# Performance work log

Hardware: AMD Instinct MI355X
Metric: run time of the kernel (lower is better)

Reference implementation:

```python
import jax, jax.numpy as jnp
import numpy as np

ROI = 268
K = 32
SLOPE = 0.33
EPS = 1e-5

def leaky(h):
    return jnp.where(h >= 0, h, SLOPE * h)

def bn(h, g, b):
    # BatchNorm in training mode: biased batch statistics over the node/batch axis
    mu = h.mean(0)
    var = ((h - mu) ** 2).mean(0)
    return (h - mu) * jax.lax.rsqrt(var + EPS) * g + b


def setup_inputs():
    B, F, C, deg = 64, ROI, 32, 32
    N = B * ROI
    key = jax.random.key(0)
    ks = jax.random.split(key, 32)
    x = jax.random.normal(ks[0], (N, F), jnp.float32)
    # static within-graph edges: every node has exactly `deg` incoming edges
    tgt = jnp.repeat(jnp.arange(N, dtype=jnp.int32), deg)
    src = (tgt // ROI) * ROI + jax.random.randint(ks[1], (N * deg,), 0, ROI, dtype=jnp.int32)
    edge_index = jnp.stack([src, tgt])
    batch = jnp.repeat(jnp.arange(B, dtype=jnp.int32), ROI)
    def lin(k, i, o):
        return 0.05 * jax.random.normal(k, (i, o), jnp.float32)
    def vec(k, o):
        return 0.05 * jax.random.normal(k, (o,), jnp.float32)
    p = dict(
        x=x, edge_index=edge_index, batch=batch,
        W1a=lin(ks[2], 2 * F, C), b1a=vec(ks[3], C), W1b=lin(ks[4], C, C), b1b=vec(ks[5], C),
        g1=1.0 + vec(ks[6], C), be1=vec(ks[7], C),
        W2a=lin(ks[8], 2 * F, C), b2a=vec(ks[9], C), W2b=lin(ks[10], C, C), b2b=vec(ks[11], C),
        g2=1.0 + vec(ks[12], C), be2=vec(ks[13], C),
        W3=lin(ks[14], 2 * F, 1), b3=vec(ks[15], 1), g3=1.0 + vec(ks[16], 1), be3=vec(ks[17], 1),
        Wl1=lin(ks[18], ROI + 2 * C, 256), bl1=vec(ks[19], 256), g4=1.0 + vec(ks[20], 256), be4=vec(ks[21], 256),
        Wl2=lin(ks[22], 256, 128), bl2=vec(ks[23], 128), g5=1.0 + vec(ks[24], 128), be5=vec(ks[25], 128),
        Wl3=lin(ks[26], 128, 1), bl3=vec(ks[27], 1),
    )
    return p


def reference(x, edge_index, batch,
              W1a, b1a, W1b, b1b, g1, be1,
              W2a, b2a, W2b, b2b, g2, be2,
              W3, b3, g3, be3,
              Wl1, bl1, g4, be4, Wl2, bl2, g5, be5, Wl3, bl3):
    N, F = x.shape
    B = N // ROI
    src, tgt = edge_index[0], edge_index[1]
    xi = x[tgt]                       # [E, F] central node feature
    xd = x[src] - xi                  # [E, F] x_j - x_i
    # --- gcn1: EdgeConv(mlp1) + BN + LeakyReLU (dropout = identity in eval) ---
    m1 = leaky(xi @ W1a[:F] + xd @ W1a[F:] + b1a) @ W1b + b1b   # [E, C]
    a1 = jax.ops.segment_max(m1, tgt, num_segments=N)
    a1 = jnp.where(jnp.isfinite(a1), a1, 0.0)
    x1 = leaky(bn(a1, g1, be1))
    # --- gcn3: EdgeConv(mlp3) + BN + LeakyReLU ---
    m3 = xi @ W3[:F] + xd @ W3[F:] + b3                          # [E, 1]
    a3 = jax.ops.segment_max(m3, tgt, num_segments=N)
    a3 = jnp.where(jnp.isfinite(a3), a3, 0.0)
    x3 = leaky(bn(a3, g3, be3))
    # --- gcn2: DynamicEdgeConv(mlp2, k=32) + BN + LeakyReLU ---
    xg = x.reshape(B, ROI, F)
    sq = jnp.sum(xg * xg, -1)
    d2 = sq[:, :, None] + sq[:, None, :] - 2.0 * jnp.einsum('bif,bjf->bij', xg, xg)
    _, idx = jax.lax.top_k(-d2, K)                               # [B, ROI, K], includes self
    xj = jax.vmap(lambda f, i: f[i])(xg, idx)                    # [B, ROI, K, F]
    part_i = jnp.einsum('bif,fc->bic', xg, W2a[:F])
    part_d = jnp.einsum('bikf,fc->bikc', xj - xg[:, :, None, :], W2a[F:])
    h2 = leaky(part_i[:, :, None, :] + part_d + b2a)
    m2 = h2 @ W2b + b2b                                          # [B, ROI, K, C]
    x2 = leaky(bn(m2.max(axis=2).reshape(N, -1), g2, be2))
    # --- readout ---
    counts = jax.ops.segment_sum(jnp.ones((N, 1), x.dtype), batch, num_segments=B)
    p1 = jax.ops.segment_sum(x1, batch, num_segments=B) / counts
    p2 = jax.ops.segment_sum(x2, batch, num_segments=B) / counts
    z = jnp.concatenate([p1, p2, x3.reshape(B, ROI)], -1)        # [B, 268+64]
    z = leaky(bn(z @ Wl1 + bl1, g4, be4))
    z = leaky(bn(z @ Wl2 + bl2, g5, be5))
    return z @ Wl3 + bl3                                          # [B, 1]
```

## Files before the change

kernel.cpp:

```cpp
#include <hip/hip_runtime.h>
#include <hip/hip_bf16.h>

#define ROI   268
#define FDIM  268
#define NB    64
#define NN    (NB*ROI)
#define CC    32
#define DEG   32
#define KSEL  32
#define SLOPE 0.33f
#define EPSBN 1e-5f

typedef __attribute__((ext_vector_type(8)))  short bf16x8;
typedef __attribute__((ext_vector_type(4)))  float f32x4;
typedef __attribute__((ext_vector_type(16))) float f32x16;

__device__ __forceinline__ float lrelu(float h) { return h >= 0.f ? h : SLOPE * h; }

__device__ __forceinline__ unsigned short f2bf(float f) {
    union { __hip_bfloat16 h; unsigned short s; } u;
    u.h = __float2bfloat16(f);
    return u.s;
}
__device__ __forceinline__ float bf2f(unsigned short h) {
    return __uint_as_float(((unsigned int)h) << 16);
}

#define PREP_PACK_BLOCKS  2448
#define PREP_PACKW_BLOCKS 18
#define PREP_SCAL_BLOCKS  1072

__global__ __launch_bounds__(256) void k_prep(
    const float* __restrict__ x,
    const float* __restrict__ W1a, const float* __restrict__ W2a,
    const float* __restrict__ W3,  const float* __restrict__ b3,
    unsigned short* __restrict__ Xh, unsigned short* __restrict__ Xl,
    unsigned short* __restrict__ Wfh, unsigned short* __restrict__ Wfl,
    float* __restrict__ u3, float* __restrict__ v3, float* __restrict__ sqv)
{
    const int bid = blockIdx.x;
    const int tid = threadIdx.x;
    if (bid < PREP_PACK_BLOCKS) {
        const int gid = bid * 256 + tid;
        const int l   = gid & 63;
        const int f3  = gid >> 6;
        const int ks  = f3 % 9;
        const int bc  = f3 / 9;
        const int ct  = bc % 17;
        const int b   = bc / 17;
        const int node = ct * 16 + (l & 15);
        const int k0   = ks * 32 + (l >> 4) * 8;
        float f[8];
        #pragma unroll
        for (int j = 0; j < 8; ++j) f[j] = 0.f;
        if (node < ROI) {
            const float* row = &x[((size_t)b * ROI + node) * FDIM];
            if (k0 + 3 < FDIM) { float4 v = *(const float4*)&row[k0];     f[0]=v.x; f[1]=v.y; f[2]=v.z; f[3]=v.w; }
            if (k0 + 7 < FDIM) { float4 v = *(const float4*)&row[k0 + 4]; f[4]=v.x; f[5]=v.y; f[6]=v.z; f[7]=v.w; }
        }
        unsigned short hh[8], ll[8];
        #pragma unroll
        for (int j = 0; j < 8; ++j) {
            hh[j] = f2bf(f[j]);
            ll[j] = f2bf(f[j] - bf2f(hh[j]));
        }
        uint4 hp, lp;
        hp.x = (unsigned)hh[0] | ((unsigned)hh[1] << 16); hp.y = (unsigned)hh[2] | ((unsigned)hh[3] << 16);
        hp.z = (unsigned)hh[4] | ((unsigned)hh[5] << 16); hp.w = (unsigned)hh[6] | ((unsigned)hh[7] << 16);
        lp.x = (unsigned)ll[0] | ((unsigned)ll[1] << 16); lp.y = (unsigned)ll[2] | ((unsigned)ll[3] << 16);
        lp.z = (unsigned)ll[4] | ((unsigned)ll[5] << 16); lp.w = (unsigned)ll[6] | ((unsigned)ll[7] << 16);
        const size_t base = (size_t)f3 * 512 + l * 8;
        *(uint4*)&Xh[base] = hp;
        *(uint4*)&Xl[base] = lp;
    } else if (bid < PREP_PACK_BLOCKS + PREP_PACKW_BLOCKS) {
        const int gid = (bid - PREP_PACK_BLOCKS) * 256 + tid;
        const int l  = gid & 63;
        const int f3 = gid >> 6;
        const int ks = f3 % 9;
        const int mc = f3 / 9;
        const int ct = mc & 1;
        const int m  = mc >> 1;
        const int k0 = ks * 32 + (l >> 4) * 8;
        const int c  = ct * 16 + (l & 15);
        const float* W = (m < 2) ? W1a : W2a;
        const bool isU = (m & 1) == 0;
        unsigned short hh[8], ll[8];
        #pragma unroll
        for (int j = 0; j < 8; ++j) {
            const int kk = k0 + j;
            float val = 0.f;
            if (kk < FDIM) {
                float wb = W[(size_t)(FDIM + kk) * CC + c];
                val = isU ? (W[(size_t)kk * CC + c] - wb) : wb;
            }
            hh[j] = f2bf(val);
            ll[j] = f2bf(val - bf2f(hh[j]));
        }
        uint4 hp, lp;
        hp.x = (unsigned)hh[0] | ((unsigned)hh[1] << 16); hp.y = (unsigned)hh[2] | ((unsigned)hh[3] << 16);
        hp.z = (unsigned)hh[4] | ((unsigned)hh[5] << 16); hp.w = (unsigned)hh[6] | ((unsigned)hh[7] << 16);
        lp.x = (unsigned)ll[0] | ((unsigned)ll[1] << 16); lp.y = (unsigned)ll[2] | ((unsigned)ll[3] << 16);
        lp.z = (unsigned)ll[4] | ((unsigned)ll[5] << 16); lp.w = (unsigned)ll[6] | ((unsigned)ll[7] << 16);
        const size_t base = (size_t)f3 * 512 + l * 8;
        *(uint4*)&Wfh[base] = hp;
        *(uint4*)&Wfl[base] = lp;
    } else {
        const int s = bid - (PREP_PACK_BLOCKS + PREP_PACKW_BLOCKS);
        const int l = tid & 63;
        #pragma unroll
        for (int i = 0; i < 4; ++i) {
            const int n = s * 16 + i * 4 + (tid >> 6);
            const float* row = &x[(size_t)n * FDIM];
            float su = 0.f, sv = 0.f, sq = 0.f;
            #pragma unroll
            for (int t = 0; t < 4; ++t) {
                const int f = l + 64 * t;
                float xv = row[f];
                float wv = W3[FDIM + f];
                float wu = W3[f] - wv;
                su += xv * wu; sv += xv * wv; sq += xv * xv;
            }
            if (l < 12) {
                const int f = 256 + l;
                float xv = row[f];
                float wv = W3[FDIM + f];
                float wu = W3[f] - wv;
                su += xv * wu; sv += xv * wv; sq += xv * xv;
            }
            #pragma unroll
            for (int mm = 32; mm > 0; mm >>= 1) {
                su += __shfl_xor(su, mm);
                sv += __shfl_xor(sv, mm);
                sq += __shfl_xor(sq, mm);
            }
            if (l == 0) {
                u3[n] = su + b3[0];
                v3[n] = sv;
                sqv[n] = sq;
            }
        }
    }
}

#define PD_DIST_BLOCKS 1088
#define PD_PROJ_BLOCKS 1088

__global__ __launch_bounds__(512) void k_projdist(
    const unsigned short* __restrict__ Xh, const unsigned short* __restrict__ Xl,
    const unsigned short* __restrict__ Wfh, const unsigned short* __restrict__ Wfl,
    const float* __restrict__ b1a, const float* __restrict__ b2a,
    const float* __restrict__ sqv,
    float* __restrict__ u1, float* __restrict__ v1,
    float* __restrict__ u2, float* __restrict__ v2,
    int* __restrict__ knn)
{
    __shared__ float S[16][297];
    __shared__ float sqj[288];
    const int tid = threadIdx.x;
    const int l   = tid & 63;
    const int w   = tid >> 6;

    if (blockIdx.x >= PD_DIST_BLOCKS) {
        const int idx  = blockIdx.x - PD_DIST_BLOCKS;
        const int b    = idx & 63;
        const int ctn  = idx >> 6;
        const int tile = b * 17 + ctn;
        const int m    = w >> 1;
        const int ct   = w & 1;
        bf16x8 Ah[9], Al[9];
        {
            const size_t abase = (size_t)tile * 9 * 512 + l * 8;
            #pragma unroll
            for (int ks = 0; ks < 9; ++ks) {
                Ah[ks] = *(const bf16x8*)&Xh[abase + ks * 512];
                Al[ks] = *(const bf16x8*)&Xl[abase + ks * 512];
            }
        }
        float* outp = (m == 0) ? u1 : (m == 1) ? v1 : (m == 2) ? u2 : v2;
        const size_t wbase = ((size_t)((m * 2 + ct) * 9)) * 512 + l * 8;
        f32x4 aHH = {0.f, 0.f, 0.f, 0.f};
        f32x4 aHL = {0.f, 0.f, 0.f, 0.f};
        f32x4 aLH = {0.f, 0.f, 0.f, 0.f};
        #pragma unroll
        for (int ks = 0; ks < 9; ++ks) {
            bf16x8 bh = *(const bf16x8*)&Wfh[wbase + ks * 512];
            bf16x8 bl = *(const bf16x8*)&Wfl[wbase + ks * 512];
            aHH = __builtin_amdgcn_mfma_f32_16x16x32_bf16(Ah[ks], bh, aHH, 0, 0, 0);
            aHL = __builtin_amdgcn_mfma_f32_16x16x32_bf16(Ah[ks], bl, aHL, 0, 0, 0);
            aLH = __builtin_amdgcn_mfma_f32_16x16x32_bf16(Al[ks], bh, aLH, 0, 0, 0);
        }
        f32x4 acc;
        #pragma unroll
        for (int i = 0; i < 4; ++i) acc[i] = (aHH[i] + aHL[i]) + aLH[i];
        const int ch = ct * 16 + (l & 15);
        float bias = 0.f;
        if (m == 0) bias = b1a[ch];
        else if (m == 2) bias = b2a[ch];
        const int r0 = (l >> 4) * 4;
        #pragma unroll
        for (int i = 0; i < 4; ++i) {
            const int node = ctn * 16 + r0 + i;
            if (node < ROI)
                outp[((size_t)b * ROI + node) * 32 + ch] = acc[i] + bias;
        }
        return;
    }

    const int bid = blockIdx.x;
    const int b   = bid & 63;
    const int rt  = bid >> 6;
    const int r0g = rt * 16;
    const int nrows = min(16, ROI - r0g);
    const size_t bN = (size_t)b * ROI;

    for (int t = tid; t < 288; t += 512)
        sqj[t] = (t < ROI) ? sqv[bN + t] : __builtin_inff();
    for (int t = tid; t < 16 * 16; t += 512)
        S[t >> 4][272 + (t & 15)] = __builtin_inff();

    bf16x8 Ah[9], Al[9];
    {
        const size_t abase = ((size_t)(b * 17 + rt) * 9) * 512 + l * 8;
        #pragma unroll
        for (int ks = 0; ks < 9; ++ks) {
            Ah[ks] = *(const bf16x8*)&Xh[abase + ks * 512];
            Al[ks] = *(const bf16x8*)&Xl[abase + ks * 512];
        }
    }
    const int rloc = (l >> 4) * 4;
    float sqr4[4];
    #pragma unroll
    for (int i = 0; i < 4; ++i) {
        const int row = r0g + rloc + i;
        sqr4[i] = (row < ROI) ? sqv[bN + row] : 0.f;
    }

    for (int ct = w; ct < 17; ct += 8) {
        const size_t bbase = ((size_t)(b * 17 + ct) * 9) * 512 + l * 8;
        f32x4 aHH = {0.f, 0.f, 0.f, 0.f};
        f32x4 aHL = {0.f, 0.f, 0.f, 0.f};
        f32x4 aLH = {0.f, 0.f, 0.f, 0.f};
        #pragma unroll
        for (int ks = 0; ks < 9; ++ks) {
            bf16x8 bh = *(const bf16x8*)&Xh[bbase + ks * 512];
            bf16x8 bl = *(const bf16x8*)&Xl[bbase + ks * 512];
            aHH = __builtin_amdgcn_mfma_f32_16x16x32_bf16(Ah[ks], bh, aHH, 0, 0, 0);
            aHL = __builtin_amdgcn_mfma_f32_16x16x32_bf16(Ah[ks], bl, aHL, 0, 0, 0);
            aLH = __builtin_amdgcn_mfma_f32_16x16x32_bf16(Al[ks], bh, aLH, 0, 0, 0);
        }
        const int col = ct * 16 + (l & 15);
        const float sj = sqj[col];
        #pragma unroll
        for (int i = 0; i < 4; ++i) {
            const float dot = (aHH[i] + aHL[i]) + aLH[i];
            S[rloc + i][col] = sqr4[i] + sj - 2.f * dot;
        }
    }
    __syncthreads();

    const int grp = tid >> 5, sl = tid & 31;
    if (grp < nrows) {
        const int row = grp;
        unsigned k[9];
        #pragma unroll
        for (int q = 0; q < 9; ++q) {
            const int idx = q * 32 + sl;
            unsigned bits = __float_as_uint(S[row][idx]);
            unsigned msk  = (unsigned)(((int)bits) >> 31) | 0x80000000u;
            k[q] = ((bits ^ msk) & ~0x1FFu) | (unsigned)idx;
        }
        #pragma unroll
        for (int i = 1; i < 9; ++i) {
            #pragma unroll
            for (int j = i; j > 0; --j) {
                unsigned lo = k[j-1] < k[j] ? k[j-1] : k[j];
                unsigned hi = k[j-1] < k[j] ? k[j]   : k[j-1];
                k[j-1] = lo; k[j] = hi;
            }
        }
        unsigned keep = 0;
        #pragma unroll
        for (int it = 0; it < KSEL; ++it) {
            unsigned m = k[0];
            #pragma unroll
            for (int mm = 16; mm > 0; mm >>= 1) {
                unsigned o = (unsigned)__shfl_xor((int)m, mm, 32);
                m = o < m ? o : m;
            }
            if (sl == it) keep = m;
            const bool win = (k[0] == m);
            #pragma unroll
            for (int q = 0; q < 8; ++q) k[q] = win ? k[q+1] : k[q];
            k[8] = win ? 0xFFFFFFFFu : k[8];
        }
        knn[(bN + r0g + row) * 32 + sl] = (int)bN + (int)(keep & 0x1FFu);
    }
}

#define EDGE_GROUPS 10
#define EDGE_NPB 27
#define VSH 40

__global__ __launch_bounds__(256) void k_edge_fused(
    const float* __restrict__ u1, const float* __restrict__ v1,
    const float* __restrict__ W1b, const float* __restrict__ b1b,
    const int* __restrict__ ei,
    const float* __restrict__ u2, const float* __restrict__ v2,
    const float* __restrict__ W2b, const float* __restrict__ b2b,
    const int* __restrict__ knn,
    const float* __restrict__ u3, const float* __restrict__ v3,
    float* __restrict__ a1, float* __restrict__ a2, float* __restrict__ a3)
{
    __shared__ __align__(16) unsigned short vs[ROI * VSH];
    __shared__ float vs3[ROI];

    const int tid  = threadIdx.x;
    const int l    = tid & 63;
    const int wv   = tid >> 6;
    const int half = l >> 5;
    const int e    = l & 31;
    const bool g1  = blockIdx.x < (NB * EDGE_GROUPS);
    const int rem  = g1 ? blockIdx.x : blockIdx.x - NB * EDGE_GROUPS;
    const int b    = rem / EDGE_GROUPS;
    const int q    = rem % EDGE_GROUPS;
    const int n0   = q * EDGE_NPB;
    const int cnt  = min(EDGE_NPB, ROI - n0);
    const size_t bN = (size_t)b * ROI;

    const float* u  = g1 ? u1 : u2;
    const float* v  = g1 ? v1 : v2;
    const float* Wb = g1 ? W1b : W2b;
    const float* bb = g1 ? b1b : b2b;
    const int* nbr  = g1 ? ei : knn;
    float* aout     = g1 ? a1 : a2;

    {
        const float* vsrc = v + bN * 32;
        for (int i = tid * 4; i < ROI * 32; i += 1024) {
            float4 vv = *(const float4*)&vsrc[i];
            const int r = i >> 5, c0 = i & 31;
            uint2 p;
            p.x = (unsigned)f2bf(vv.x) | ((unsigned)f2bf(vv.y) << 16);
            p.y = (unsigned)f2bf(vv.z) | ((unsigned)f2bf(vv.w) << 16);
            *(uint2*)&vs[r * VSH + c0] = p;
        }
        if (g1)
            for (int t = tid; t < ROI; t += 256) vs3[t] = v3[bN + t];
    }

    union { bf16x8 v8; unsigned u4[4]; } B0, B1;
    #pragma unroll
    for (int j = 0; j < 4; ++j) {
        B0.u4[j] = (unsigned)f2bf(Wb[(half * 8 + 2*j    ) * 32 + e])
                 | ((unsigned)f2bf(Wb[(half * 8 + 2*j + 1) * 32 + e]) << 16);
        B1.u4[j] = (unsigned)f2bf(Wb[(16 + half * 8 + 2*j    ) * 32 + e])
                 | ((unsigned)f2bf(Wb[(16 + half * 8 + 2*j + 1) * 32 + e]) << 16);
    }
    const float biasc = bb[e];

    int jns[8];
    {
        const int nper = (cnt + 3) >> 2;
        #pragma unroll
        for (int s = 0; s < 8; ++s) jns[s] = 0;
        for (int s = 0; s < nper; ++s) {
            const int il = wv + s * 4;
            if (il < cnt)
                jns[s] = nbr[(size_t)((int)bN + n0 + il) * DEG + e] - (int)bN;
        }
    }
    __syncthreads();

    int s = 0;
    for (int il = wv; il < cnt; il += 4, ++s) {
        const int n   = (int)bN + n0 + il;
        const int jnl = jns[s];

        float hv[16];
        #pragma unroll
        for (int ss = 0; ss < 2; ++ss) {
            const int c0 = ss * 16 + half * 8;
            float4 uv0 = *(const float4*)&u[(size_t)n * 32 + c0];
            float4 uv1 = *(const float4*)&u[(size_t)n * 32 + c0 + 4];
            bf16x8 vb = *(const bf16x8*)&vs[jnl * VSH + c0];
            const unsigned short* vbs = (const unsigned short*)&vb;
            hv[ss*8+0] = lrelu(uv0.x + bf2f(vbs[0]));
            hv[ss*8+1] = lrelu(uv0.y + bf2f(vbs[1]));
            hv[ss*8+2] = lrelu(uv0.z + bf2f(vbs[2]));
            hv[ss*8+3] = lrelu(uv0.w + bf2f(vbs[3]));
            hv[ss*8+4] = lrelu(uv1.x + bf2f(vbs[4]));
            hv[ss*8+5] = lrelu(uv1.y + bf2f(vbs[5]));
            hv[ss*8+6] = lrelu(uv1.z + bf2f(vbs[6]));
            hv[ss*8+7] = lrelu(uv1.w + bf2f(vbs[7]));
        }
        union { bf16x8 v8; unsigned u4[4]; } A0, A1;
        #pragma unroll
        for (int j = 0; j < 4; ++j) {
            A0.u4[j] = (unsigned)f2bf(hv[2*j])     | ((unsigned)f2bf(hv[2*j + 1]) << 16);
            A1.u4[j] = (unsigned)f2bf(hv[8 + 2*j]) | ((unsigned)f2bf(hv[8 + 2*j + 1]) << 16);
        }
        f32x16 acc = {0.f,0.f,0.f,0.f,0.f,0.f,0.f,0.f,0.f,0.f,0.f,0.f,0.f,0.f,0.f,0.f};
        acc = __builtin_amdgcn_mfma_f32_32x32x16_bf16(A0.v8, B0.v8, acc, 0, 0, 0);
        acc = __builtin_amdgcn_mfma_f32_32x32x16_bf16(A1.v8, B1.v8, acc, 0, 0, 0);

        float mx = acc[0];
        #pragma unroll
        for (int r = 1; r < 16; ++r) mx = fmaxf(mx, acc[r]);
        mx = fmaxf(mx, __shfl_xor(mx, 32));
        if (l < 32) aout[(size_t)n * 32 + l] = mx + biasc;

        if (g1) {
            float a3v = u3[n] + vs3[jnl];
            #pragma unroll
            for (int mm = 16; mm > 0; mm >>= 1) a3v = fmaxf(a3v, __shfl_xor(a3v, mm));
            if (l == 0) a3[n] = a3v;
        }
    }
}

__global__ __launch_bounds__(256) void k_stats1(
    const float* __restrict__ a1, const float* __restrict__ a2,
    float* __restrict__ part)
{
    const int p = blockIdx.x;
    const int tid = threadIdx.x;
    const int ch = tid & 31, sub = tid >> 5;
    const size_t base = (size_t)p * ROI;
    float s1 = 0.f, q1 = 0.f, s2 = 0.f, q2 = 0.f;
    for (int n = sub; n < ROI; n += 8) {
        float v1 = a1[(base + n) * 32 + ch];
        float v2 = a2[(base + n) * 32 + ch];
        s1 += v1; q1 += v1 * v1; s2 += v2; q2 += v2 * v2;
    }
    __shared__ float L[4][256];
    L[0][tid] = s1; L[1][tid] = q1; L[2][tid] = s2; L[3][tid] = q2;
    __syncthreads();
    if (tid < 128) {
        const int a = tid >> 5, c = tid & 31;
        float s = 0.f;
        #pragma unroll
        for (int k = 0; k < 8; ++k) s += L[a][c + 32 * k];
        part[p * 128 + a * 32 + c] = s;
    }
}

__global__ __launch_bounds__(256) void k_pool_fc1(
    const float* __restrict__ a1, const float* __restrict__ a2, const float* __restrict__ a3,
    const float* __restrict__ part,
    const float* __restrict__ g1, const float* __restrict__ be1,
    const float* __restrict__ g2, const float* __restrict__ be2,
    const float* __restrict__ g3, const float* __restrict__ be3,
    const float* __restrict__ Wl1, const float* __restrict__ bl1,
    float* __restrict__ h1)
{
    const int b = blockIdx.x, tid = threadIdx.x;
    __shared__ float stl[130];
    __shared__ float zs[332];
    __shared__ float P[4][64];
    __shared__ float S3[256], Q3[256];

    {
        float p0 = 0.f, p1 = 0.f, p2 = 0.f, p3 = 0.f;
        float q0 = 0.f, q1 = 0.f, q2 = 0.f, q3 = 0.f;
        int n = tid;
        for (; n + 768 < NN; n += 1024) {
            float a = a3[n], bb = a3[n + 256], c = a3[n + 512], d = a3[n + 768];
            p0 += a; q0 += a * a;
            p1 += bb; q1 += bb * bb;
            p2 += c; q2 += c * c;
            p3 += d; q3 += d * d;
        }
        for (; n < NN; n += 256) { float a = a3[n]; p0 += a; q0 += a * a; }
        S3[tid] = (p0 + p1) + (p2 + p3);
        Q3[tid] = (q0 + q1) + (q2 + q3);
    }
    __syncthreads();
    for (int off = 128; off > 0; off >>= 1) {
        if (tid < off) { S3[tid] += S3[tid + off]; Q3[tid] += Q3[tid + off]; }
        __syncthreads();
    }
    if (tid < 64) {
        const int a = (tid >> 5) * 2, c = tid & 31;
        float s0 = 0.f, s1 = 0.f, q0b = 0.f, q1b = 0.f;
        for (int p = 0; p < 64; p += 2) {
            s0  += part[p * 128 + a * 32 + c];
            q0b += part[p * 128 + (a + 1) * 32 + c];
            s1  += part[(p + 1) * 128 + a * 32 + c];
            q1b += part[(p + 1) * 128 + (a + 1) * 32 + c];
        }
        float ss = s0 + s1, qq = q0b + q1b;
        float gv = (tid < 32) ? g1[c] : g2[c];
        float bv = (tid < 32) ? be1[c] : be2[c];
        float mu  = ss * (1.f / NN);
        float var = qq * (1.f / NN) - mu * mu;
        float sc  = gv * rsqrtf(var + EPSBN);
        stl[tid * 2] = sc; stl[tid * 2 + 1] = bv - mu * sc;
    }
    if (tid == 64) {
        float mu  = S3[0] * (1.f / NN);
        float var = Q3[0] * (1.f / NN) - mu * mu;
        float sc  = g3[0] * rsqrtf(var + EPSBN);
        stl[128] = sc; stl[129] = be3[0] - mu * sc;
    }
    __syncthreads();

    const int c = tid & 63, grp = tid >> 6;
    const float* src = (c < 32) ? a1 : a2;
    const int ch = c & 31;
    const float sc = stl[c * 2], sh = stl[c * 2 + 1];
    {
        const size_t rb = (size_t)b * ROI;
        float p0 = 0.f, p1 = 0.f, p2 = 0.f, p3 = 0.f;
        int i = grp;
        for (; i + 12 < ROI; i += 16) {
            p0 += lrelu(src[(rb + i)      * 32 + ch] * sc + sh);
            p1 += lrelu(src[(rb + i + 4)  * 32 + ch] * sc + sh);
            p2 += lrelu(src[(rb + i + 8)  * 32 + ch] * sc + sh);
            p3 += lrelu(src[(rb + i + 12) * 32 + ch] * sc + sh);
        }
        for (; i < ROI; i += 4)
            p0 += lrelu(src[(rb + i) * 32 + ch] * sc + sh);
        P[grp][c] = (p0 + p1) + (p2 + p3);
    }
    const float sc3 = stl[128], sh3 = stl[129];
    for (int i = tid; i < ROI; i += 256)
        zs[64 + i] = lrelu(a3[b * ROI + i] * sc3 + sh3);
    __syncthreads();
    if (tid < 64)
        zs[tid] = (P[0][tid] + P[1][tid] + P[2][tid] + P[3][tid]) * (1.f / ROI);
    __syncthreads();

    {
        float s0 = 0.f, s1 = 0.f, s2 = 0.f, s3 = 0.f;
        #pragma unroll 4
        for (int k = 0; k < 332; k += 4) {
            s0 += zs[k]     * Wl1[(size_t)k       * 256 + tid];
            s1 += zs[k + 1] * Wl1[(size_t)(k + 1) * 256 + tid];
            s2 += zs[k + 2] * Wl1[(size_t)(k + 2) * 256 + tid];
            s3 += zs[k + 3] * Wl1[(size_t)(k + 3) * 256 + tid];
        }
        h1[(size_t)b * 256 + tid] = bl1[tid] + ((s0 + s1) + (s2 + s3));
    }
}

__global__ __launch_bounds__(128) void k_fc2s(
    const float* __restrict__ h1,
    const float* __restrict__ g4, const float* __restrict__ be4,
    const float* __restrict__ Wl2, const float* __restrict__ bl2,
    float* __restrict__ h2)
{
    const int b = blockIdx.x, tid = threadIdx.x;
    __shared__ float hs[256];
    float s0 = 0.f, q0 = 0.f, s1 = 0.f, q1 = 0.f;
    float s2 = 0.f, q2 = 0.f, s3 = 0.f, q3 = 0.f;
    for (int r = 0; r < NB; r += 2) {
        float a = h1[(size_t)r * 256 + tid];
        float c = h1[(size_t)r * 256 + tid + 128];
        float d = h1[(size_t)(r + 1) * 256 + tid];
        float e = h1[(size_t)(r + 1) * 256 + tid + 128];
        s0 += a; q0 += a * a;
        s1 += c; q1 += c * c;
        s2 += d; q2 += d * d;
        s3 += e; q3 += e * e;
    }
    {
        float ssA = s0 + s2, qqA = q0 + q2;
        float muA = ssA * (1.f / NB);
        float vaA = qqA * (1.f / NB) - muA * muA;
        float scA = g4[tid] * rsqrtf(vaA + EPSBN);
        float shA = be4[tid] - muA * scA;
        hs[tid] = lrelu(h1[(size_t)b * 256 + tid] * scA + shA);
        float ssB = s1 + s3, qqB = q1 + q3;
        float muB = ssB * (1.f / NB);
        float vaB = qqB * (1.f / NB) - muB * muB;
        float scB = g4[tid + 128] * rsqrtf(vaB + EPSBN);
        float shB = be4[tid + 128] - muB * scB;
        hs[tid + 128] = lrelu(h1[(size_t)b * 256 + tid + 128] * scB + shB);
    }
    __syncthreads();
    float s0b = 0.f, s1b = 0.f, s2b = 0.f, s3b = 0.f;
    #pragma unroll 4
    for (int k = 0; k < 256; k += 4) {
        s0b += hs[k]     * Wl2[(size_t)k       * 128 + tid];
        s1b += hs[k + 1] * Wl2[(size_t)(k + 1) * 128 + tid];
        s2b += hs[k + 2] * Wl2[(size_t)(k + 2) * 128 + tid];
        s3b += hs[k + 3] * Wl2[(size_t)(k + 3) * 128 + tid];
    }
    h2[(size_t)b * 128 + tid] = bl2[tid] + ((s0b + s1b) + (s2b + s3b));
}

__global__ __launch_bounds__(128) void k_fc3s(
    const float* __restrict__ h2,
    const float* __restrict__ g5, const float* __restrict__ be5,
    const float* __restrict__ Wl3, const float* __restrict__ bl3,
    float* __restrict__ out)
{
    const int tid = threadIdx.x;
    __shared__ float T[64][133];
    float s0 = 0.f, q0 = 0.f, s1 = 0.f, q1 = 0.f;
    for (int r = 0; r < NB; r += 2) {
        float a = h2[(size_t)r * 128 + tid];
        float b = h2[(size_t)(r + 1) * 128 + tid];
        s0 += a; q0 += a * a;
        s1 += b; q1 += b * b;
    }
    float ss = s0 + s1, qq = q0 + q1;
    float mu  = ss * (1.f / NB);
    float var = qq * (1.f / NB) - mu * mu;
    float sc  = g5[tid] * rsqrtf(var + EPSBN);
    float sh  = be5[tid] - mu * sc;
    const float w3 = Wl3[tid];
    for (int r = 0; r < NB; ++r)
        T[r][tid] = lrelu(h2[(size_t)r * 128 + tid] * sc + sh) * w3;
    __syncthreads();
    if (tid < 64) {
        float a0 = 0.f, a1 = 0.f, a2 = 0.f, a3 = 0.f;
        #pragma unroll 4
        for (int c = 0; c < 128; c += 4) {
            a0 += T[tid][c];
            a1 += T[tid][c + 1];
            a2 += T[tid][c + 2];
            a3 += T[tid][c + 3];
        }
        out[tid] = bl3[0] + ((a0 + a1) + (a2 + a3));
    }
}

extern "C" void kernel_launch(void* const* d_in, const int* in_sizes, int n_in,
                              void* d_out, int out_size, void* d_ws, size_t ws_size,
                              hipStream_t stream)
{
    (void)in_sizes; (void)n_in; (void)out_size; (void)ws_size;
    const float* x   = (const float*)d_in[0];
    const int*   ei  = (const int*)d_in[1];
    const float* W1a = (const float*)d_in[3];
    const float* b1a = (const float*)d_in[4];
    const float* W1b = (const float*)d_in[5];
    const float* b1b = (const float*)d_in[6];
    const float* g1  = (const float*)d_in[7];
    const float* be1 = (const float*)d_in[8];
    const float* W2a = (const float*)d_in[9];
    const float* b2a = (const float*)d_in[10];
    const float* W2b = (const float*)d_in[11];
    const float* b2b = (const float*)d_in[12];
    const float* g2  = (const float*)d_in[13];
    const float* be2 = (const float*)d_in[14];
    const float* W3  = (const float*)d_in[15];
    const float* b3  = (const float*)d_in[16];
    const float* g3  = (const float*)d_in[17];
    const float* be3 = (const float*)d_in[18];
    const float* Wl1 = (const float*)d_in[19];
    const float* bl1 = (const float*)d_in[20];
    const float* g4  = (const float*)d_in[21];
    const float* be4 = (const float*)d_in[22];
    const float* Wl2 = (const float*)d_in[23];
    const float* bl2 = (const float*)d_in[24];
    const float* g5  = (const float*)d_in[25];
    const float* be5 = (const float*)d_in[26];
    const float* Wl3 = (const float*)d_in[27];
    const float* bl3 = (const float*)d_in[28];

    float* ws  = (float*)d_ws;
    float* u1  = ws;
    float* v1  = u1 + (size_t)NN * 32;
    float* u2  = v1 + (size_t)NN * 32;
    float* v2  = u2 + (size_t)NN * 32;
    float* u3  = v2 + (size_t)NN * 32;
    float* v3  = u3 + NN;
    float* sqv = v3 + NN;
    float* a1  = sqv + NN;
    float* a2  = a1 + (size_t)NN * 32;
    float* a3  = a2 + (size_t)NN * 32;
    float* h1  = a3 + NN;
    float* h2  = h1 + (size_t)NB * 256;
    float* part = h2 + (size_t)NB * 128;
    int*   knn = (int*)(part + 64 * 128);
    unsigned short* Xh = (unsigned short*)(((uintptr_t)(knn + (size_t)NN * 32) + 255) & ~(uintptr_t)255);
    unsigned short* Xl = Xh + (size_t)64 * 17 * 9 * 512;
    unsigned short* Wfh = Xl + (size_t)64 * 17 * 9 * 512;
    unsigned short* Wfl = Wfh + (size_t)8 * 9 * 512;

    k_prep<<<PREP_PACK_BLOCKS + PREP_PACKW_BLOCKS + PREP_SCAL_BLOCKS, 256, 0, stream>>>(
        x, W1a, W2a, W3, b3, Xh, Xl, Wfh, Wfl, u3, v3, sqv);
    k_projdist<<<PD_DIST_BLOCKS + PD_PROJ_BLOCKS, 512, 0, stream>>>(
        Xh, Xl, Wfh, Wfl, b1a, b2a, sqv, u1, v1, u2, v2, knn);
    k_edge_fused<<<2 * NB * EDGE_GROUPS, 256, 0, stream>>>(
        u1, v1, W1b, b1b, ei, u2, v2, W2b, b2b, knn, u3, v3, a1, a2, a3);
    k_stats1<<<64, 256, 0, stream>>>(a1, a2, part);
    k_pool_fc1<<<NB, 256, 0, stream>>>(a1, a2, a3, part, g1, be1, g2, be2, g3, be3,
                                       Wl1, bl1, h1);
    k_fc2s<<<NB, 128, 0, stream>>>(h1, g4, be4, Wl2, bl2, h2);
    k_fc3s<<<1, 128, 0, stream>>>(h2, g5, be5, Wl3, bl3, (float*)d_out);
}
```

Baseline: 133.9 us.

## Process 32 distance rows per block with interleaved dual-row top-k selection

```diff
diff --git a/kernel.cpp b/kernel.cpp
--- a/kernel.cpp
+++ b/kernel.cpp
@@ -142,7 +142,7 @@
     }
 }
 
-#define PD_DIST_BLOCKS 1088
+#define PD_DIST_BLOCKS 576
 #define PD_PROJ_BLOCKS 1088
 
 __global__ __launch_bounds__(512) void k_projdist(
@@ -154,7 +154,7 @@
     float* __restrict__ u2, float* __restrict__ v2,
     int* __restrict__ knn)
 {
-    __shared__ float S[16][297];
+    __shared__ float S[32][297];
     __shared__ float sqj[288];
     const int tid = threadIdx.x;
     const int l   = tid & 63;
@@ -209,25 +209,27 @@
     const int bid = blockIdx.x;
     const int b   = bid & 63;
     const int rt  = bid >> 6;
-    const int r0g = rt * 16;
-    const int nrows = min(16, ROI - r0g);
+    const int r0g = rt * 32;
+    const int nrows = min(32, ROI - r0g);
     const size_t bN = (size_t)b * ROI;
 
     for (int t = tid; t < 288; t += 512)
         sqj[t] = (t < ROI) ? sqv[bN + t] : __builtin_inff();
-    for (int t = tid; t < 16 * 16; t += 512)
+    for (int t = tid; t < 32 * 16; t += 512)
         S[t >> 4][272 + (t & 15)] = __builtin_inff();
 
+    const int a  = w & 1;
+    const int at = min(rt * 2 + a, 16);
     bf16x8 Ah[9], Al[9];
     {
-        const size_t abase = ((size_t)(b * 17 + rt) * 9) * 512 + l * 8;
+        const size_t abase = ((size_t)(b * 17 + at) * 9) * 512 + l * 8;
         #pragma unroll
         for (int ks = 0; ks < 9; ++ks) {
             Ah[ks] = *(const bf16x8*)&Xh[abase + ks * 512];
             Al[ks] = *(const bf16x8*)&Xl[abase + ks * 512];
         }
     }
-    const int rloc = (l >> 4) * 4;
+    const int rloc = (at - rt * 2) * 16 + (l >> 4) * 4;
     float sqr4[4];
     #pragma unroll
     for (int i = 0; i < 4; ++i) {
@@ -235,7 +237,7 @@
         sqr4[i] = (row < ROI) ? sqv[bN + row] : 0.f;
     }
 
-    for (int ct = w; ct < 17; ct += 8) {
+    for (int ct = (w >> 1); ct < 17; ct += 4) {
         const size_t bbase = ((size_t)(b * 17 + ct) * 9) * 512 + l * 8;
         f32x4 aHH = {0.f, 0.f, 0.f, 0.f};
         f32x4 aHL = {0.f, 0.f, 0.f, 0.f};
@@ -259,42 +261,56 @@
     __syncthreads();
 
     const int grp = tid >> 5, sl = tid & 31;
-    if (grp < nrows) {
-        const int row = grp;
-        unsigned k[9];
-        #pragma unroll
-        for (int q = 0; q < 9; ++q) {
-            const int idx = q * 32 + sl;
-            unsigned bits = __float_as_uint(S[row][idx]);
-            unsigned msk  = (unsigned)(((int)bits) >> 31) | 0x80000000u;
-            k[q] = ((bits ^ msk) & ~0x1FFu) | (unsigned)idx;
-        }
-        #pragma unroll
-        for (int i = 1; i < 9; ++i) {
-            #pragma unroll
-            for (int j = i; j > 0; --j) {
-                unsigned lo = k[j-1] < k[j] ? k[j-1] : k[j];
-                unsigned hi = k[j-1] < k[j] ? k[j]   : k[j-1];
-                k[j-1] = lo; k[j] = hi;
-            }
-        }
-        unsigned keep = 0;
-        #pragma unroll
-        for (int it = 0; it < KSEL; ++it) {
-            unsigned m = k[0];
-            #pragma unroll
-            for (int mm = 16; mm > 0; mm >>= 1) {
-                unsigned o = (unsigned)__shfl_xor((int)m, mm, 32);
-                m = o < m ? o : m;
-            }
-            if (sl == it) keep = m;
-            const bool win = (k[0] == m);
-            #pragma unroll
-            for (int q = 0; q < 8; ++q) k[q] = win ? k[q+1] : k[q];
-            k[8] = win ? 0xFFFFFFFFu : k[8];
-        }
-        knn[(bN + r0g + row) * 32 + sl] = (int)bN + (int)(keep & 0x1FFu);
-    }
+    const int rowA = grp, rowB = grp + 16;
+    unsigned ka[9], kb[9];
+    #pragma unroll
+    for (int q = 0; q < 9; ++q) {
+        const int idx = q * 32 + sl;
+        unsigned ba = __float_as_uint(S[rowA][idx]);
+        unsigned ma = (unsigned)(((int)ba) >> 31) | 0x80000000u;
+        ka[q] = ((ba ^ ma) & ~0x1FFu) | (unsigned)idx;
+        unsigned bb = __float_as_uint(S[rowB][idx]);
+        unsigned mb = (unsigned)(((int)bb) >> 31) | 0x80000000u;
+        kb[q] = ((bb ^ mb) & ~0x1FFu) | (unsigned)idx;
+    }
+    #pragma unroll
+    for (int i = 1; i < 9; ++i) {
+        #pragma unroll
+        for (int j = i; j > 0; --j) {
+            unsigned loA = ka[j-1] < ka[j] ? ka[j-1] : ka[j];
+            unsigned hiA = ka[j-1] < ka[j] ? ka[j]   : ka[j-1];
+            ka[j-1] = loA; ka[j] = hiA;
+            unsigned loB = kb[j-1] < kb[j] ? kb[j-1] : kb[j];
+            unsigned hiB = kb[j-1] < kb[j] ? kb[j]   : kb[j-1];
+            kb[j-1] = loB; kb[j] = hiB;
+        }
+    }
+    unsigned keepA = 0, keepB = 0;
+    #pragma unroll
+    for (int it = 0; it < KSEL; ++it) {
+        unsigned mA = ka[0], mB = kb[0];
+        #pragma unroll
+        for (int mm = 16; mm > 0; mm >>= 1) {
+            unsigned oA = (unsigned)__shfl_xor((int)mA, mm, 32);
+            unsigned oB = (unsigned)__shfl_xor((int)mB, mm, 32);
+            mA = oA < mA ? oA : mA;
+            mB = oB < mB ? oB : mB;
+        }
+        if (sl == it) { keepA = mA; keepB = mB; }
+        const bool winA = (ka[0] == mA);
+        const bool winB = (kb[0] == mB);
+        #pragma unroll
+        for (int q = 0; q < 8; ++q) {
+            ka[q] = winA ? ka[q+1] : ka[q];
+            kb[q] = winB ? kb[q+1] : kb[q];
+        }
+        ka[8] = winA ? 0xFFFFFFFFu : ka[8];
+        kb[8] = winB ? 0xFFFFFFFFu : kb[8];
+    }
+    if (rowA < nrows)
+        knn[(bN + r0g + rowA) * 32 + sl] = (int)bN + (int)(keepA & 0x1FFu);
+    if (rowB < nrows)
+        knn[(bN + r0g + rowB) * 32 + sl] = (int)bN + (int)(keepB & 0x1FFu);
 }
 
 #define EDGE_GROUPS 10
```

Result: no change. 131.4 us, median of 3 (-1.8%).
